# Optimization experiments

Hardware: AMD Instinct MI355X
Metric: run time of the kernel (lower is better)

The kernel has to match this reference:

```python
import jax, jax.numpy as jnp
import numpy as np

N = 50000      # nodes (single coalesced node type)
IN = 256       # in_dim
H = 8          # attention heads
D = 64         # hidden_dim (per-head out dim)
HD = H * D     # 512, fused feature dim
OUT = 64       # final out_dim
M = 2          # meta-paths
E = 800000     # edges per meta-path graph
SEM_HID = 128  # SemanticAttention hidden size (DGL/OpenHGNN default)
NEG_SLOPE = 0.2


def setup_inputs() -> dict:
    key = jax.random.key(0)
    ks = jax.random.split(key, 13)
    s = 0.05
    return {
        "x": jax.random.normal(ks[0], (N, IN), jnp.float32),
        "src": jax.random.randint(ks[1], (M, E), 0, N, jnp.int32),
        "dst": jax.random.randint(ks[2], (M, E), 0, N, jnp.int32),
        # per-metapath GATConv params
        "Wg": jax.random.normal(ks[3], (M, IN, HD), jnp.float32) * s,
        "al": jax.random.normal(ks[4], (M, H, D), jnp.float32) * s,
        "ar": jax.random.normal(ks[5], (M, H, D), jnp.float32) * s,
        "bg": jax.random.normal(ks[6], (M, HD), jnp.float32) * s,
        # semantic attention: Linear(HD,128) -> tanh -> Linear(128,1,no bias)
        "W1": jax.random.normal(ks[7], (HD, SEM_HID), jnp.float32) * s,
        "b1": jax.random.normal(ks[8], (SEM_HID,), jnp.float32) * s,
        "q": jax.random.normal(ks[9], (SEM_HID,), jnp.float32) * s,
        # final linear
        "Wout": jax.random.normal(ks[10], (HD, OUT), jnp.float32) * s,
        "bout": jax.random.normal(ks[11], (OUT,), jnp.float32) * s,
    }


def _gat(x, W, al, ar, b, src, dst):
    # x: [N, IN] -> feat: [N, H, D]
    feat = (x @ W).reshape(N, H, D)
    el = jnp.sum(feat * al, axis=-1)                      # [N, H]
    er = jnp.sum(feat * ar, axis=-1)                      # [N, H]
    e = jax.nn.leaky_relu(el[src] + er[dst], NEG_SLOPE)   # [E, H]
    # edge softmax per destination node (allow zero in-degree)
    m = jax.ops.segment_max(e, dst, num_segments=N)       # [N, H]
    m = jnp.where(jnp.isfinite(m), m, 0.0)
    ex = jnp.exp(e - m[dst])                              # [E, H]
    den = jax.ops.segment_sum(ex, dst, num_segments=N)    # [N, H]
    alpha = ex / jnp.maximum(den[dst], 1e-9)              # [E, H]
    # scatter-aggregate messages: [E, H, D] -> [N, H, D]
    out = jax.ops.segment_sum(alpha[:, :, None] * feat[src], dst, num_segments=N)
    return jax.nn.elu(out.reshape(N, HD) + b)             # flatten heads + bias + elu


def reference(x, src, dst, Wg, al, ar, bg, W1, b1, q, Wout, bout):
    # per-metapath GAT (loop over M=2 structurally distinct graphs)
    zs = [_gat(x, Wg[p], al[p], ar[p], bg[p], src[p], dst[p]) for p in range(M)]
    z = jnp.stack(zs, axis=1)                             # [N, M, HD]
    # semantic attention fusion
    w = jnp.mean(jnp.tanh(z @ W1 + b1) @ q, axis=0)       # [M]
    beta = jax.nn.softmax(w)                              # [M]
    fused = jnp.einsum("nmf,m->nf", z, beta)             # [N, HD]
    # final linear
    return fused @ Wout + bout                            # [N, OUT]
```

## Files before the change

kernel.cpp:

```cpp
#include <hip/hip_runtime.h>
#include <cstdint>

#define N_NODES 50000
#define IN_DIM 256
#define H_HEADS 8
#define D_HEAD 64
#define HD 512
#define OUT_DIM 64
#define M_PATHS 2
#define E_EDGES 800000
#define SEM_HID 128
#define NEG_SLOPE 0.2f
#define ELL_CAP 64

typedef __attribute__((ext_vector_type(8))) short bf16x8;
typedef __attribute__((ext_vector_type(4))) float f32x4;
typedef __attribute__((ext_vector_type(8))) unsigned short u16x8;

__device__ __forceinline__ float b2f(unsigned short u) {
  return __uint_as_float(((unsigned)u) << 16);
}
__device__ __forceinline__ unsigned short f2b(float f) {
  unsigned u = __float_as_uint(f);
  unsigned r = (u + 0x7fffu + ((u >> 16) & 1u)) >> 16;
  return (unsigned short)r;
}

__device__ __forceinline__ float eluf(float x) {
  return x > 0.f ? x : (expf(x) - 1.f);
}
__device__ __forceinline__ float lrelu(float x) {
  return x > 0.f ? x : NEG_SLOPE * x;
}

__global__ void k_prep(const float* __restrict__ Wg, const float* __restrict__ W1,
                       const float* __restrict__ Wout, const float* __restrict__ al,
                       const float* __restrict__ ar,
                       unsigned short* __restrict__ WgbT, unsigned short* __restrict__ W1T,
                       unsigned short* __restrict__ WoutT, unsigned short* __restrict__ WALR,
                       int* __restrict__ deg2, float* __restrict__ wsem) {
  int gid = blockIdx.x * blockDim.x + threadIdx.x;
  if (gid < 262144) {
    int m = gid >> 17, r = gid & 131071, n = r >> 8, k = r & 255;
    WgbT[(size_t)m * 131072 + n * 256 + k] = f2b(Wg[(size_t)m * 131072 + k * 512 + n]);
  } else if (gid < 327680) {
    int r = gid - 262144; int c = r >> 9, k = r & 511;
    W1T[c * 512 + k] = f2b(W1[k * 128 + c]);
  } else if (gid < 360448) {
    int r = gid - 327680; int c = r >> 9, k = r & 511;
    WoutT[c * 512 + k] = f2b(Wout[k * 64 + c]);
  } else if (gid < 368640) {
    int r = gid - 360448;
    int c = r >> 8, k = r & 255;
    int m = c >> 4, side = (c >> 3) & 1, h = c & 7;
    const float* av = (side ? ar : al) + m * HD + h * D_HEAD;
    const float* wrow = Wg + (size_t)m * 131072 + (size_t)k * HD + h * D_HEAD;
    float s = 0.f;
#pragma unroll
    for (int d = 0; d < 64; ++d) s += wrow[d] * av[d];
    WALR[c * 256 + k] = f2b(s);
  } else if (gid < 468640) {
    deg2[gid - 368640] = 0;
  } else if (gid < 468642) {
    wsem[gid - 468640] = 0.f;
  }
}

__global__ __launch_bounds__(256) void k_elx(const float* __restrict__ xfp,
                                             const unsigned short* __restrict__ WALR,
                                             unsigned short* __restrict__ xb,
                                             float* __restrict__ el2,
                                             float* __restrict__ er2) {
  __shared__ __align__(16) unsigned short As[64][72];
  __shared__ __align__(16) unsigned short Bs[32][72];
  const int tid = threadIdx.x;
  const int r0 = blockIdx.x * 64;
  const int w = tid >> 6, lane = tid & 63;
  const int cl = lane & 15, kg = lane >> 4;
  f32x4 acc[2] = {};
  for (int k0 = 0; k0 < IN_DIM; k0 += 64) {
#pragma unroll
    for (int p = 0; p < 2; ++p) {
      int idx = tid + p * 256;
      int row = idx >> 3, ko = (idx & 7) * 8;
      u16x8 v = (u16x8)(unsigned short)0;
      int grow = r0 + row;
      if (grow < N_NODES) {
        const float4* g = (const float4*)&xfp[(size_t)grow * IN_DIM + k0 + ko];
        float4 g0 = g[0], g1 = g[1];
        v[0] = f2b(g0.x); v[1] = f2b(g0.y); v[2] = f2b(g0.z); v[3] = f2b(g0.w);
        v[4] = f2b(g1.x); v[5] = f2b(g1.y); v[6] = f2b(g1.z); v[7] = f2b(g1.w);
        *(u16x8*)&xb[(size_t)grow * IN_DIM + k0 + ko] = v;
      }
      *(u16x8*)&As[row][ko] = v;
    }
    {
      int col = tid >> 3, ko = (tid & 7) * 8;
      *(u16x8*)&Bs[col][ko] = *(const u16x8*)&WALR[col * 256 + k0 + ko];
    }
    __syncthreads();
#pragma unroll
    for (int kk = 0; kk < 64; kk += 32) {
      bf16x8 a = *(const bf16x8*)&As[w * 16 + cl][kk + kg * 8];
#pragma unroll
      for (int ct = 0; ct < 2; ++ct) {
        bf16x8 b = *(const bf16x8*)&Bs[ct * 16 + cl][kk + kg * 8];
        acc[ct] = __builtin_amdgcn_mfma_f32_16x16x32_bf16(a, b, acc[ct], 0, 0, 0);
      }
    }
    __syncthreads();
  }
#pragma unroll
  for (int ct = 0; ct < 2; ++ct) {
    int col = ct * 16 + cl;
    int m = col >> 4, side = (col >> 3) & 1, h = col & 7;
    float* dstp = (side ? er2 : el2) + m * 400000;
#pragma unroll
    for (int reg = 0; reg < 4; ++reg) {
      int row = r0 + w * 16 + kg * 4 + reg;
      if (row < N_NODES) dstp[row * 8 + h] = acc[ct][reg];
    }
  }
}

__global__ void k_edge_e(const int* __restrict__ src, const int* __restrict__ dst,
                         int* __restrict__ deg, unsigned short* __restrict__ ell_src) {
  int e = blockIdx.x * blockDim.x + threadIdx.x;
  if (e >= E_EDGES) return;
  int d = dst[e];
  int p = atomicAdd(&deg[d], 1);
  if (p < ELL_CAP) ell_src[d * ELL_CAP + p] = (unsigned short)src[e];
}

__global__ __launch_bounds__(256) void k_gemm_feat(const unsigned short* __restrict__ xb,
                                                   const unsigned short* __restrict__ BT,
                                                   unsigned short* __restrict__ C) {
  __shared__ __align__(16) unsigned short As[64][72];
  __shared__ __align__(16) unsigned short Bs[256][72];
  const int tid = threadIdx.x;
  const int r0 = blockIdx.x * 64, c0 = blockIdx.y * 256;
  const int w = tid >> 6, lane = tid & 63;
  const int cl = lane & 15, kg = lane >> 4;
  const int rw = (w >> 1) * 32;
  const int cw = (w & 1) * 128;
  f32x4 acc[2][8] = {};
  for (int k0 = 0; k0 < IN_DIM; k0 += 64) {
#pragma unroll
    for (int p = 0; p < 2; ++p) {
      int idx = tid + p * 256;
      int row = idx >> 3, ko = (idx & 7) * 8;
      u16x8 v = (u16x8)(unsigned short)0;
      int grow = r0 + row;
      if (grow < N_NODES) v = *(const u16x8*)&xb[(size_t)grow * IN_DIM + k0 + ko];
      *(u16x8*)&As[row][ko] = v;
    }
#pragma unroll
    for (int p = 0; p < 8; ++p) {
      int idx = tid + p * 256;
      int col = idx >> 3, ko = (idx & 7) * 8;
      *(u16x8*)&Bs[col][ko] = *(const u16x8*)&BT[(size_t)(c0 + col) * IN_DIM + k0 + ko];
    }
    __syncthreads();
#pragma unroll
    for (int kk = 0; kk < 64; kk += 32) {
      bf16x8 a0 = *(const bf16x8*)&As[rw + cl][kk + kg * 8];
      bf16x8 a1 = *(const bf16x8*)&As[rw + 16 + cl][kk + kg * 8];
#pragma unroll
      for (int ct = 0; ct < 8; ++ct) {
        bf16x8 b = *(const bf16x8*)&Bs[cw + ct * 16 + cl][kk + kg * 8];
        acc[0][ct] = __builtin_amdgcn_mfma_f32_16x16x32_bf16(a0, b, acc[0][ct], 0, 0, 0);
        acc[1][ct] = __builtin_amdgcn_mfma_f32_16x16x32_bf16(a1, b, acc[1][ct], 0, 0, 0);
      }
    }
    __syncthreads();
  }
  const int ccol = c0 + cw;
#pragma unroll
  for (int rt = 0; rt < 2; ++rt)
#pragma unroll
    for (int ct = 0; ct < 8; ++ct)
#pragma unroll
      for (int reg = 0; reg < 4; ++reg) {
        int row = r0 + rw + rt * 16 + kg * 4 + reg;
        if (row < N_NODES) C[(size_t)row * HD + ccol + ct * 16 + cl] = f2b(acc[rt][ct][reg]);
      }
}

__global__ __launch_bounds__(256) void k_agg(const unsigned short* __restrict__ featb,
                                             const float* __restrict__ el,
                                             const float* __restrict__ er,
                                             const unsigned short* __restrict__ ell_src,
                                             const int* __restrict__ deg,
                                             const float* __restrict__ bg,
                                             unsigned short* __restrict__ z) {
  __shared__ float lds_ex[4][544];
  const int tid = threadIdx.x;
  const int widx = tid >> 6, lane = tid & 63;
  const int n = blockIdx.x * 4 + widx;
  const int h = lane >> 3;
  int s_raw = (int)ell_src[n * ELL_CAP + lane];
  int dcnt_raw = deg[n];
  const float4* r4 = (const float4*)&er[n * 8];
  float4 b0 = r4[0], b1v = r4[1];
  int s_reg = s_raw;
  const float4* e4 = (const float4*)&el[s_reg * 8];
  float4 a0 = e4[0], a1 = e4[1];
  const int dcnt = min(dcnt_raw, ELL_CAP);
  const bool valid = lane < dcnt;
  float evf[8];
  evf[0] = lrelu(a0.x + b0.x); evf[1] = lrelu(a0.y + b0.y);
  evf[2] = lrelu(a0.z + b0.z); evf[3] = lrelu(a0.w + b0.w);
  evf[4] = lrelu(a1.x + b1v.x); evf[5] = lrelu(a1.y + b1v.y);
  evf[6] = lrelu(a1.z + b1v.z); evf[7] = lrelu(a1.w + b1v.w);
  if (!valid) {
#pragma unroll
    for (int j = 0; j < 8; ++j) evf[j] = -1e30f;
  }
  float mx[8];
#pragma unroll
  for (int j = 0; j < 8; ++j) mx[j] = evf[j];
#pragma unroll
  for (int off = 1; off < 64; off <<= 1)
#pragma unroll
    for (int j = 0; j < 8; ++j) mx[j] = fmaxf(mx[j], __shfl_xor(mx[j], off));
#pragma unroll
  for (int j = 0; j < 8; ++j) {
    float exv = valid ? expf(evf[j] - mx[j]) : 0.f;
    lds_ex[widx][j * 68 + lane] = exv;
  }
  float acc[8] = {};
  float densum = 0.f;
  const float* exrow = &lds_ex[widx][h * 68];
  const unsigned short* fb = featb + lane * 8;
  int i = 0;
  for (; i + 8 <= dcnt; i += 8) {
    int ss[8];
    float ww[8];
    u16x8 ff[8];
#pragma unroll
    for (int u = 0; u < 8; ++u) {
      ss[u] = __shfl(s_reg, i + u);
      ww[u] = exrow[i + u];
    }
#pragma unroll
    for (int u = 0; u < 8; ++u) ff[u] = *(const u16x8*)&fb[(size_t)ss[u] * HD];
#pragma unroll
    for (int u = 0; u < 8; ++u) {
      densum += ww[u];
#pragma unroll
      for (int j = 0; j < 8; ++j) acc[j] += ww[u] * b2f(ff[u][j]);
    }
  }
  for (; i + 4 <= dcnt; i += 4) {
    int ss[4];
    float ww[4];
    u16x8 ff[4];
#pragma unroll
    for (int u = 0; u < 4; ++u) {
      ss[u] = __shfl(s_reg, i + u);
      ww[u] = exrow[i + u];
    }
#pragma unroll
    for (int u = 0; u < 4; ++u) ff[u] = *(const u16x8*)&fb[(size_t)ss[u] * HD];
#pragma unroll
    for (int u = 0; u < 4; ++u) {
      densum += ww[u];
#pragma unroll
      for (int j = 0; j < 8; ++j) acc[j] += ww[u] * b2f(ff[u][j]);
    }
  }
  for (; i < dcnt; ++i) {
    int s0 = __shfl(s_reg, i);
    float w0 = exrow[i];
    u16x8 f0 = *(const u16x8*)&fb[(size_t)s0 * HD];
    densum += w0;
#pragma unroll
    for (int j = 0; j < 8; ++j) acc[j] += w0 * b2f(f0[j]);
  }
  float ds = 1.f / fmaxf(densum, 1e-9f);
  const float4* bg4 = (const float4*)&bg[lane * 8];
  float4 bga = bg4[0], bgb = bg4[1];
  float bgv[8] = {bga.x, bga.y, bga.z, bga.w, bgb.x, bgb.y, bgb.z, bgb.w};
  u16x8 zo;
#pragma unroll
  for (int j = 0; j < 8; ++j) zo[j] = f2b(eluf(acc[j] * ds + bgv[j]));
  *(u16x8*)&z[(size_t)n * HD + lane * 8] = zo;
}

__global__ __launch_bounds__(256) void k_gemm_post(const unsigned short* __restrict__ Zb,
                                                   const unsigned short* __restrict__ W1T,
                                                   const unsigned short* __restrict__ WoutT,
                                                   const float* __restrict__ b1,
                                                   const float* __restrict__ qv,
                                                   float* __restrict__ wsem_m,
                                                   unsigned short* __restrict__ yb) {
  __shared__ __align__(16) unsigned short As[128][72];
  __shared__ __align__(16) unsigned short Bs[192][72];
  __shared__ float redv[16];
  const int tid = threadIdx.x;
  const int r0 = blockIdx.x * 128;
  const int w = tid >> 6, lane = tid & 63;
  const int cl = lane & 15, kg = lane >> 4;
  const int rw = w * 32;
  f32x4 acc[2][12] = {};
  for (int k0 = 0; k0 < HD; k0 += 64) {
#pragma unroll
    for (int p = 0; p < 4; ++p) {
      int idx = tid + p * 256;
      int row = idx >> 3, ko = (idx & 7) * 8;
      u16x8 v = (u16x8)(unsigned short)0;
      if (r0 + row < N_NODES) v = *(const u16x8*)&Zb[(size_t)(r0 + row) * HD + k0 + ko];
      *(u16x8*)&As[row][ko] = v;
    }
#pragma unroll
    for (int p = 0; p < 6; ++p) {
      int idx = tid + p * 256;
      int col = idx >> 3, ko = (idx & 7) * 8;
      u16x8 v = (col < 128) ? *(const u16x8*)&W1T[(size_t)col * HD + k0 + ko]
                            : *(const u16x8*)&WoutT[(size_t)(col - 128) * HD + k0 + ko];
      *(u16x8*)&Bs[col][ko] = v;
    }
    __syncthreads();
#pragma unroll
    for (int kk = 0; kk < 64; kk += 32) {
      bf16x8 a0 = *(const bf16x8*)&As[rw + cl][kk + kg * 8];
      bf16x8 a1 = *(const bf16x8*)&As[rw + 16 + cl][kk + kg * 8];
#pragma unroll
      for (int ct = 0; ct < 12; ++ct) {
        bf16x8 b = *(const bf16x8*)&Bs[ct * 16 + cl][kk + kg * 8];
        acc[0][ct] = __builtin_amdgcn_mfma_f32_16x16x32_bf16(a0, b, acc[0][ct], 0, 0, 0);
        acc[1][ct] = __builtin_amdgcn_mfma_f32_16x16x32_bf16(a1, b, acc[1][ct], 0, 0, 0);
      }
    }
    __syncthreads();
  }
  float rs[2][4] = {};
#pragma unroll
  for (int ct = 0; ct < 8; ++ct) {
    int col = ct * 16 + cl;
    float bb = b1[col], qq = qv[col];
#pragma unroll
    for (int rt = 0; rt < 2; ++rt)
#pragma unroll
      for (int reg = 0; reg < 4; ++reg)
        rs[rt][reg] += tanhf(acc[rt][ct][reg] + bb) * qq;
  }
#pragma unroll
  for (int off = 1; off < 16; off <<= 1)
#pragma unroll
    for (int rt = 0; rt < 2; ++rt)
#pragma unroll
      for (int reg = 0; reg < 4; ++reg) rs[rt][reg] += __shfl_xor(rs[rt][reg], off);
  float val = 0.f;
#pragma unroll
  for (int rt = 0; rt < 2; ++rt)
#pragma unroll
    for (int reg = 0; reg < 4; ++reg) {
      int row = r0 + rw + rt * 16 + kg * 4 + reg;
      if (row < N_NODES) val += rs[rt][reg];
    }
  if (cl == 0) redv[w * 4 + kg] = val;
  __syncthreads();
  if (tid == 0) {
    float sv = 0.f;
#pragma unroll
    for (int k = 0; k < 16; ++k) sv += redv[k];
    atomicAdd(wsem_m, sv);
  }
#pragma unroll
  for (int rt = 0; rt < 2; ++rt)
#pragma unroll
    for (int ct = 8; ct < 12; ++ct)
#pragma unroll
      for (int reg = 0; reg < 4; ++reg) {
        int row = r0 + rw + rt * 16 + kg * 4 + reg;
        if (row < N_NODES)
          yb[(size_t)row * OUT_DIM + (ct - 8) * 16 + cl] = f2b(acc[rt][ct][reg]);
      }
}

__global__ void k_final(const unsigned short* __restrict__ yb, const float* __restrict__ wsem,
                        const float* __restrict__ bout, float* __restrict__ out) {
  int gid = blockIdx.x * blockDim.x + threadIdx.x;
  size_t off = (size_t)gid * 8;
  if (off >= (size_t)N_NODES * OUT_DIM) return;
  float w0 = wsem[0] / (float)N_NODES, w1 = wsem[1] / (float)N_NODES;
  float mxv = fmaxf(w0, w1);
  float e0 = expf(w0 - mxv), e1 = expf(w1 - mxv);
  float inv = 1.f / (e0 + e1);
  float b0 = e0 * inv, b1v = e1 * inv;
  u16x8 ya = *(const u16x8*)&yb[off];
  u16x8 yc = *(const u16x8*)&yb[(size_t)N_NODES * OUT_DIM + off];
  const int cb = (int)(off & 63);
#pragma unroll
  for (int j = 0; j < 8; ++j)
    out[off + j] = b0 * b2f(ya[j]) + b1v * b2f(yc[j]) + bout[cb + j];
}

extern "C" void kernel_launch(void* const* d_in, const int* in_sizes, int n_in,
                              void* d_out, int out_size, void* d_ws, size_t ws_size,
                              hipStream_t stream) {
  const float* x    = (const float*)d_in[0];
  const int*   src  = (const int*)d_in[1];
  const int*   dst  = (const int*)d_in[2];
  const float* Wg   = (const float*)d_in[3];
  const float* al   = (const float*)d_in[4];
  const float* ar   = (const float*)d_in[5];
  const float* bg   = (const float*)d_in[6];
  const float* W1   = (const float*)d_in[7];
  const float* b1   = (const float*)d_in[8];
  const float* q    = (const float*)d_in[9];
  const float* Wout = (const float*)d_in[10];
  const float* bout = (const float*)d_in[11];
  float* out = (float*)d_out;

  char* ws = (char*)d_ws;
  unsigned short* featb = (unsigned short*)(ws);
  unsigned short* z     = (unsigned short*)(ws + 51200000);
  unsigned short* yb    = (unsigned short*)(ws + 102400000);
  unsigned short* xb    = (unsigned short*)(ws + 115200000);
  unsigned short* ell   = (unsigned short*)(ws + 140800000);
  float* el2            = (float*)(ws + 147200000);
  float* er2            = (float*)(ws + 150400000);
  int* deg2             = (int*)(ws + 153600000);
  unsigned short* WgbT  = (unsigned short*)(ws + 154000000);
  unsigned short* W1T   = (unsigned short*)(ws + 154524288);
  unsigned short* WoutT = (unsigned short*)(ws + 154655360);
  unsigned short* WALR  = (unsigned short*)(ws + 154720896);
  float* wsem           = (float*)(ws + 154737280);

  k_prep<<<1831, 256, 0, stream>>>(Wg, W1, Wout, al, ar, WgbT, W1T, WoutT, WALR,
                                   deg2, wsem);
  k_elx<<<782, 256, 0, stream>>>(x, WALR, xb, el2, er2);

  for (int m = 0; m < M_PATHS; ++m) {
    const int* srcm = src + (size_t)m * E_EDGES;
    const int* dstm = dst + (size_t)m * E_EDGES;
    k_edge_e<<<3125, 256, 0, stream>>>(srcm, dstm, deg2 + m * N_NODES, ell);
    dim3 gf(782, 2);
    k_gemm_feat<<<gf, 256, 0, stream>>>(xb, WgbT + (size_t)m * 131072, featb);
    k_agg<<<12500, 256, 0, stream>>>(featb, el2 + m * 400000, er2 + m * 400000,
                                     ell, deg2 + m * N_NODES, bg + m * HD, z);
    k_gemm_post<<<391, 256, 0, stream>>>(z, W1T, WoutT, b1, q, wsem + m,
                                         yb + (size_t)m * N_NODES * OUT_DIM);
  }
  k_final<<<1563, 256, 0, stream>>>(yb, wsem, bout, out);
}
```

Measured before the change: 551.5 us.

## Switch features to head-major layout and parallelize aggregation over heads

Stores projected features, el/er and z in head-major planes ([H][N][64]) instead of node-major rows. The aggregation kernel now launches one block per (node group, head), so each wave handles one head and one destination node. Each wave gathers 8 edges at once, each with a 128-byte row, then reduces across lane groups. The aim is to shrink each head's gather working set for better cache locality and to remove the LDS staging of softmax weights. The cost is 8x more blocks, a cross-lane reduction per wave, repeated index and deg loads per head, and strided loads in the post GEMM.

```diff
diff --git a/kernel.cpp b/kernel.cpp
--- a/kernel.cpp
+++ b/kernel.cpp
@@ -12,6 +12,7 @@
 #define SEM_HID 128
 #define NEG_SLOPE 0.2f
 #define ELL_CAP 64
+#define HN 3200000
 
 typedef __attribute__((ext_vector_type(8))) short bf16x8;
 typedef __attribute__((ext_vector_type(4))) float f32x4;
@@ -114,11 +115,11 @@
   for (int ct = 0; ct < 2; ++ct) {
     int col = ct * 16 + cl;
     int m = col >> 4, side = (col >> 3) & 1, h = col & 7;
-    float* dstp = (side ? er2 : el2) + m * 400000;
+    float* dstp = (side ? er2 : el2) + m * 400000 + h * N_NODES;
 #pragma unroll
     for (int reg = 0; reg < 4; ++reg) {
       int row = r0 + w * 16 + kg * 4 + reg;
-      if (row < N_NODES) dstp[row * 8 + h] = acc[ct][reg];
+      if (row < N_NODES) dstp[row] = acc[ct][reg];
     }
   }
 }
@@ -182,7 +183,10 @@
 #pragma unroll
       for (int reg = 0; reg < 4; ++reg) {
         int row = r0 + rw + rt * 16 + kg * 4 + reg;
-        if (row < N_NODES) C[(size_t)row * HD + ccol + ct * 16 + cl] = f2b(acc[rt][ct][reg]);
+        int col = ccol + ct * 16 + cl;
+        int h = col >> 6, d = col & 63;
+        if (row < N_NODES)
+          C[(size_t)h * HN + (size_t)row * 64 + d] = f2b(acc[rt][ct][reg]);
       }
 }
 
@@ -193,98 +197,62 @@
                                              const int* __restrict__ deg,
                                              const float* __restrict__ bg,
                                              unsigned short* __restrict__ z) {
-  __shared__ float lds_ex[4][544];
   const int tid = threadIdx.x;
   const int widx = tid >> 6, lane = tid & 63;
-  const int n = blockIdx.x * 4 + widx;
-  const int h = lane >> 3;
+  const int bid = blockIdx.x;
+  const int h = bid & 7;
+  const int n = (bid >> 3) * 4 + widx;
+  int dcnt = min(deg[n], ELL_CAP);
   int s_raw = (int)ell_src[n * ELL_CAP + lane];
-  int dcnt_raw = deg[n];
-  const float4* r4 = (const float4*)&er[n * 8];
-  float4 b0 = r4[0], b1v = r4[1];
-  int s_reg = s_raw;
-  const float4* e4 = (const float4*)&el[s_reg * 8];
-  float4 a0 = e4[0], a1 = e4[1];
-  const int dcnt = min(dcnt_raw, ELL_CAP);
+  int s_reg = min(s_raw, N_NODES - 1);
+  float sc = lrelu(el[(size_t)h * N_NODES + s_reg] + er[(size_t)h * N_NODES + n]);
   const bool valid = lane < dcnt;
-  float evf[8];
-  evf[0] = lrelu(a0.x + b0.x); evf[1] = lrelu(a0.y + b0.y);
-  evf[2] = lrelu(a0.z + b0.z); evf[3] = lrelu(a0.w + b0.w);
-  evf[4] = lrelu(a1.x + b1v.x); evf[5] = lrelu(a1.y + b1v.y);
-  evf[6] = lrelu(a1.z + b1v.z); evf[7] = lrelu(a1.w + b1v.w);
-  if (!valid) {
-#pragma unroll
-    for (int j = 0; j < 8; ++j) evf[j] = -1e30f;
-  }
-  float mx[8];
-#pragma unroll
-  for (int j = 0; j < 8; ++j) mx[j] = evf[j];
-#pragma unroll
-  for (int off = 1; off < 64; off <<= 1)
-#pragma unroll
-    for (int j = 0; j < 8; ++j) mx[j] = fmaxf(mx[j], __shfl_xor(mx[j], off));
-#pragma unroll
-  for (int j = 0; j < 8; ++j) {
-    float exv = valid ? expf(evf[j] - mx[j]) : 0.f;
-    lds_ex[widx][j * 68 + lane] = exv;
-  }
+  if (!valid) sc = -1e30f;
+  float mxv = sc;
+#pragma unroll
+  for (int off = 1; off < 64; off <<= 1) mxv = fmaxf(mxv, __shfl_xor(mxv, off));
+  float ex = valid ? expf(sc - mxv) : 0.f;
+  float den = ex;
+#pragma unroll
+  for (int off = 1; off < 64; off <<= 1) den += __shfl_xor(den, off);
+  const float ds = 1.f / fmaxf(den, 1e-9f);
+  const int g = lane >> 3;
+  const int dlo = (lane & 7) * 8;
+  const unsigned short* fbh = featb + (size_t)h * HN + dlo;
   float acc[8] = {};
-  float densum = 0.f;
-  const float* exrow = &lds_ex[widx][h * 68];
-  const unsigned short* fb = featb + lane * 8;
   int i = 0;
-  for (; i + 8 <= dcnt; i += 8) {
-    int ss[8];
-    float ww[8];
-    u16x8 ff[8];
-#pragma unroll
-    for (int u = 0; u < 8; ++u) {
-      ss[u] = __shfl(s_reg, i + u);
-      ww[u] = exrow[i + u];
-    }
-#pragma unroll
-    for (int u = 0; u < 8; ++u) ff[u] = *(const u16x8*)&fb[(size_t)ss[u] * HD];
-#pragma unroll
-    for (int u = 0; u < 8; ++u) {
-      densum += ww[u];
-#pragma unroll
-      for (int j = 0; j < 8; ++j) acc[j] += ww[u] * b2f(ff[u][j]);
-    }
-  }
-  for (; i + 4 <= dcnt; i += 4) {
-    int ss[4];
-    float ww[4];
-    u16x8 ff[4];
-#pragma unroll
-    for (int u = 0; u < 4; ++u) {
-      ss[u] = __shfl(s_reg, i + u);
-      ww[u] = exrow[i + u];
-    }
-#pragma unroll
-    for (int u = 0; u < 4; ++u) ff[u] = *(const u16x8*)&fb[(size_t)ss[u] * HD];
-#pragma unroll
-    for (int u = 0; u < 4; ++u) {
-      densum += ww[u];
-#pragma unroll
-      for (int j = 0; j < 8; ++j) acc[j] += ww[u] * b2f(ff[u][j]);
-    }
-  }
-  for (; i < dcnt; ++i) {
-    int s0 = __shfl(s_reg, i);
-    float w0 = exrow[i];
-    u16x8 f0 = *(const u16x8*)&fb[(size_t)s0 * HD];
-    densum += w0;
+  for (; i + 16 <= dcnt; i += 16) {
+    int e0 = i + g, e1 = i + 8 + g;
+    float w0 = __shfl(ex, e0);
+    float w1 = __shfl(ex, e1);
+    int s0 = __shfl(s_reg, e0);
+    int s1 = __shfl(s_reg, e1);
+    u16x8 f0 = *(const u16x8*)&fbh[(size_t)s0 * 64];
+    u16x8 f1 = *(const u16x8*)&fbh[(size_t)s1 * 64];
 #pragma unroll
     for (int j = 0; j < 8; ++j) acc[j] += w0 * b2f(f0[j]);
-  }
-  float ds = 1.f / fmaxf(densum, 1e-9f);
-  const float4* bg4 = (const float4*)&bg[lane * 8];
-  float4 bga = bg4[0], bgb = bg4[1];
-  float bgv[8] = {bga.x, bga.y, bga.z, bga.w, bgb.x, bgb.y, bgb.z, bgb.w};
-  u16x8 zo;
-#pragma unroll
-  for (int j = 0; j < 8; ++j) zo[j] = f2b(eluf(acc[j] * ds + bgv[j]));
-  *(u16x8*)&z[(size_t)n * HD + lane * 8] = zo;
+#pragma unroll
+    for (int j = 0; j < 8; ++j) acc[j] += w1 * b2f(f1[j]);
+  }
+  for (; i < dcnt; i += 8) {
+    int e0 = i + g;
+    float w0 = __shfl(ex, e0);
+    int s0 = __shfl(s_reg, e0);
+    u16x8 f0 = *(const u16x8*)&fbh[(size_t)s0 * 64];
+#pragma unroll
+    for (int j = 0; j < 8; ++j) acc[j] += w0 * b2f(f0[j]);
+  }
+#pragma unroll
+  for (int off = 8; off < 64; off <<= 1)
+#pragma unroll
+    for (int j = 0; j < 8; ++j) acc[j] += __shfl_xor(acc[j], off);
+  if (g == 0) {
+    u16x8 zo;
+#pragma unroll
+    for (int j = 0; j < 8; ++j)
+      zo[j] = f2b(eluf(acc[j] * ds + bg[h * 64 + dlo + j]));
+    *(u16x8*)&z[(size_t)h * HN + (size_t)n * 64 + dlo] = zo;
+  }
 }
 
 __global__ __launch_bounds__(256) void k_gemm_post(const unsigned short* __restrict__ Zb,
@@ -308,8 +276,10 @@
     for (int p = 0; p < 4; ++p) {
       int idx = tid + p * 256;
       int row = idx >> 3, ko = (idx & 7) * 8;
+      int kc = k0 + ko, hh = kc >> 6, dd = kc & 63;
       u16x8 v = (u16x8)(unsigned short)0;
-      if (r0 + row < N_NODES) v = *(const u16x8*)&Zb[(size_t)(r0 + row) * HD + k0 + ko];
+      if (r0 + row < N_NODES)
+        v = *(const u16x8*)&Zb[(size_t)hh * HN + (size_t)(r0 + row) * 64 + dd];
       *(u16x8*)&As[row][ko] = v;
     }
 #pragma unroll
@@ -439,8 +409,8 @@
     k_edge_e<<<3125, 256, 0, stream>>>(srcm, dstm, deg2 + m * N_NODES, ell);
     dim3 gf(782, 2);
     k_gemm_feat<<<gf, 256, 0, stream>>>(xb, WgbT + (size_t)m * 131072, featb);
-    k_agg<<<12500, 256, 0, stream>>>(featb, el2 + m * 400000, er2 + m * 400000,
-                                     ell, deg2 + m * N_NODES, bg + m * HD, z);
+    k_agg<<<100000, 256, 0, stream>>>(featb, el2 + m * 400000, er2 + m * 400000,
+                                      ell, deg2 + m * N_NODES, bg + m * HD, z);
     k_gemm_post<<<391, 256, 0, stream>>>(z, W1T, WoutT, b1, q, wsem + m,
                                          yb + (size_t)m * N_NODES * OUT_DIM);
   }
```

Result: slower. 719.3 us (+30.4%).
